# Kernel tuning notes

Measured on AMD Instinct MI355X. Metric: run time of the kernel, lower is better.

Reference implementation:

```python
import jax, jax.numpy as jnp
import numpy as np

B, S, N, F, H, O = 4, 16, 1024, 64, 128, 64
L_LAYERS, N_HEADS, CHUNK = 3, 4, 128
EPS = 1e-5


def setup_inputs() -> dict:
    key = jax.random.key(0)
    ks = jax.random.split(key, 16)
    adj = (jax.random.uniform(ks[0], (B, S, N, N)) < 0.05).astype(jnp.float32)
    adj = adj * (1.0 - jnp.eye(N, dtype=jnp.float32))
    x = jax.random.normal(ks[1], (B, S, F), dtype=jnp.float32)
    mask = jnp.ones((B, S), dtype=jnp.float32)
    sd = lambda fan_in: 1.0 / np.sqrt(fan_in)
    inp = {
        "x": x, "adj": adj, "mask": mask,
        "feature_importance": jnp.ones((F,), jnp.float32),
        "W_in": jax.random.normal(ks[2], (F, H)) * sd(F),
        "b_in": jnp.zeros((H,), jnp.float32),
        "ln_g": jnp.ones((H,), jnp.float32),
        "ln_b": jnp.zeros((H,), jnp.float32),
        "gcn_W": jax.random.normal(ks[3], (L_LAYERS, H, H)) * sd(H),
        "gcn_b": jnp.zeros((L_LAYERS, H), jnp.float32),
        "bn_g": jnp.ones((L_LAYERS, H), jnp.float32),
        "bn_b": jnp.zeros((L_LAYERS, H), jnp.float32),
        "Wqkv": jax.random.normal(ks[4], (3 * H, H)) * sd(H),
        "bqkv": jnp.zeros((3 * H,), jnp.float32),
        "Wo": jax.random.normal(ks[5], (H, H)) * sd(H),
        "bo": jnp.zeros((H,), jnp.float32),
        "W_out": jax.random.normal(ks[6], (H, O)) * sd(H),
        "b_out": jnp.zeros((O,), jnp.float32),
    }
    return inp


def _chunked_mha(h, Wqkv, bqkv, Wo, bo):
    # h: [B,S,N,H]; attention within chunks of CHUNK nodes (torch MHA, eval mode)
    b, s, n, hdim = h.shape
    c, dh = n // CHUNK, hdim // N_HEADS
    xr = h.reshape(b, s, c, CHUNK, hdim)
    qkv = xr @ Wqkv.T + bqkv                      # [B,S,C,L,3H]
    q, k, v = jnp.split(qkv, 3, axis=-1)
    split = lambda t: t.reshape(b, s, c, CHUNK, N_HEADS, dh).swapaxes(-3, -2)  # [B,S,C,nh,L,dh]
    q, k, v = split(q) * (dh ** -0.5), split(k), split(v)
    attn = jax.nn.softmax(jnp.einsum('bscnld,bscnmd->bscnlm', q, k), axis=-1)
    o = jnp.einsum('bscnlm,bscnmd->bscnld', attn, v)
    o = o.swapaxes(-3, -2).reshape(b, s, c, CHUNK, hdim) @ Wo.T + bo
    return o.reshape(b, s, n, hdim)


def reference(x, adj, mask, feature_importance, W_in, b_in, ln_g, ln_b,
              gcn_W, gcn_b, bn_g, bn_b, Wqkv, bqkv, Wo, bo, W_out, b_out):
    b, s, f = x.shape
    n = adj.shape[-1]
    # feature scaling + input projection + layer norm (same vector for all nodes)
    xv = (x * feature_importance) @ W_in + b_in            # [B,S,H]
    mu = xv.mean(-1, keepdims=True)
    var = ((xv - mu) ** 2).mean(-1, keepdims=True)
    hv = (xv - mu) / jnp.sqrt(var + EPS) * ln_g + ln_b
    h = jnp.broadcast_to(hv[:, :, None, :], (b, s, n, hv.shape[-1]))  # [B,S,N,H]
    h_init = h
    # GCN normalization: D^{-1/2} (A + I) D^{-1/2}
    A_hat = adj + jnp.eye(n, dtype=adj.dtype)
    dinv = jax.lax.rsqrt(A_hat.sum(-1))                     # [B,S,N]
    A_norm = dinv[..., :, None] * A_hat * dinv[..., None, :]
    bn_scale = 1.0 / np.sqrt(1.0 + EPS)  # eval BN, running mean 0 / var 1
    for l in range(L_LAYERS):
        hw = h @ gcn_W[l]
        hc = jnp.einsum('bsnm,bsmh->bsnh', A_norm, hw) + gcn_b[l]
        hc = hc * bn_scale * bn_g[l] + bn_b[l]
        hc = _chunked_mha(hc, Wqkv, bqkv, Wo, bo)
        hc = jax.nn.relu(hc)  # dropout = identity in eval
        h = h + hc            # use_skip (num_layers > 1)
    h = h + h_init
    node_embeddings = h @ W_out + b_out                    # [B,S,N,O]
    graph_embeddings = node_embeddings.mean(axis=2)        # [B,S,O]
    graph_embeddings = graph_embeddings * mask[:, :, None]
    node_embeddings = node_embeddings * mask[:, :, None, None]
    return node_embeddings, graph_embeddings
```

## Files before the change

### kernel.cpp

```cpp
#include <hip/hip_runtime.h>

typedef __bf16 bf16_t;
typedef bf16_t bf16x8 __attribute__((ext_vector_type(8)));
typedef float f32x4 __attribute__((ext_vector_type(4)));

#define DEV static __device__ __forceinline__

constexpr float kBnScale = 0.999995000037499375f;

DEV unsigned short f2bf(float f) {
  unsigned u = __builtin_bit_cast(unsigned, f);
  u += 0x7fffu + ((u >> 16) & 1u);
  return (unsigned short)(u >> 16);
}
DEV float bf2f(unsigned short s) {
  return __builtin_bit_cast(float, ((unsigned)s) << 16);
}
DEV f32x4 mfma16(bf16x8 a, bf16x8 b, f32x4 c) {
  return __builtin_amdgcn_mfma_f32_16x16x32_bf16(a, b, c, 0, 0, 0);
}
DEV unsigned swz(unsigned byteoff, unsigned row) { return byteoff ^ ((row & 7u) << 4); }

__global__ __launch_bounds__(256) void k_pre(
    const float* __restrict__ adj, unsigned short* __restrict__ cols,
    int* __restrict__ cnt, float* __restrict__ dinv,
    const float* __restrict__ x, const float* __restrict__ fi,
    const float* __restrict__ Win, const float* __restrict__ bin,
    const float* __restrict__ lng, const float* __restrict__ lnb,
    const float* __restrict__ gW, const float* __restrict__ bng,
    float* __restrict__ hv, float* __restrict__ hw0s,
    const float* __restrict__ Wqkv, const float* __restrict__ Wo,
    const float* __restrict__ Wout,
    unsigned short* __restrict__ WqkvB, unsigned short* __restrict__ WoB,
    unsigned short* __restrict__ gWB, unsigned short* __restrict__ WoutB) {
  const int bid = blockIdx.x;
  if (bid < 16384) {
    const int c4 = (bid & 7) * 2048 + (bid >> 3);
    const int w = threadIdx.x >> 6, lane = threadIdx.x & 63;
    const long row = (long)c4 * 4 + w;
    const float* ap = adj + row * 1024;
    unsigned short* cp = cols + row * 128;
    int c = 0;
#pragma unroll
    for (int it = 0; it < 4; ++it) {
      const float4 v4 = *(const float4*)(ap + it * 256 + lane * 4);
      const float vv[4] = {v4.x, v4.y, v4.z, v4.w};
#pragma unroll
      for (int j = 0; j < 4; ++j) {
        const unsigned long long m = __ballot(vv[j] != 0.0f);
        const int pos = c + __popcll(m & ((1ull << lane) - 1ull));
        if (vv[j] != 0.0f && pos < 128) cp[pos] = (unsigned short)(it * 256 + lane * 4 + j);
        c += __popcll(m);
      }
    }
    if (lane == 0) {
      cnt[row] = c;
      dinv[row] = 1.0f / sqrtf((float)(c + 1));
    }
  } else if (bid < 16448) {
    __shared__ float sred[2], sred2[2], shv[128];
    const int bs = bid - 16384, t = threadIdx.x;
    float accv = 0.f, d = 0.f;
    if (t < 128) {
      accv = bin[t];
      for (int f = 0; f < 64; ++f) accv += x[bs * 64 + f] * fi[f] * Win[f * 128 + t];
      float ssum = accv;
      for (int m = 1; m < 64; m <<= 1) ssum += __shfl_xor(ssum, m);
      if ((t & 63) == 0) sred[t >> 6] = ssum;
    }
    __syncthreads();
    const float mu = (sred[0] + sred[1]) * (1.0f / 128.0f);
    if (t < 128) {
      d = accv - mu;
      float vs = d * d;
      for (int m = 1; m < 64; m <<= 1) vs += __shfl_xor(vs, m);
      if ((t & 63) == 0) sred2[t >> 6] = vs;
    }
    __syncthreads();
    const float var = (sred2[0] + sred2[1]) * (1.0f / 128.0f);
    if (t < 128) {
      const float h = d / sqrtf(var + 1e-5f) * lng[t] + lnb[t];
      hv[bs * 128 + t] = h;
      shv[t] = h;
    }
    __syncthreads();
    if (t < 128) {
      float a2 = 0.f;
      for (int k = 0; k < 128; ++k) a2 += shv[k] * gW[k * 128 + t];
      hw0s[bs * 128 + t] = a2 * kBnScale * bng[t];
    }
  } else {
    const int i = (bid - 16448) * 256 + threadIdx.x;
    if (i < 49152) {
      WqkvB[i] = f2bf(Wqkv[i]);
    } else if (i < 65536) {
      const int j = i - 49152;
      WoB[j] = f2bf(Wo[j]);
    } else if (i < 114688) {
      const int j = i - 65536, l = j >> 14, r = j & 16383, n = r >> 7, k = r & 127;
      gWB[j] = f2bf(gW[(l << 14) + k * 128 + n]);
    } else {
      const int j = i - 114688, n = j >> 7, k = j & 127;
      WoutB[j] = f2bf(Wout[k * 64 + n]);
    }
  }
}

__global__ __launch_bounds__(256) void k_scal2(const unsigned short* __restrict__ cols,
                                               const int* __restrict__ cnt, const float* __restrict__ dinv,
                                               const float* __restrict__ hw0s,
                                               const float* __restrict__ gb0, const float* __restrict__ bng0,
                                               const float* __restrict__ bnb0,
                                               unsigned* __restrict__ hc0) {
  int b = blockIdx.x;
  b = (b & 7) * 2048 + (b >> 3);
  const int w = threadIdx.x >> 6, lane = threadIdx.x & 63;
  const long row = (long)b * 4 + w;
  const int cn = cnt[row] < 128 ? cnt[row] : 128;
  const long bsbase = row & ~1023L;
  const int c0 = cols[row * 128 + lane];
  const int c1 = cols[row * 128 + 64 + lane];
  float s = 0.f;
  if (lane < cn) s += dinv[bsbase + c0];
  if (lane + 64 < cn) s += dinv[bsbase + c1];
  for (int m = 1; m < 64; m <<= 1) s += __shfl_xor(s, m);
  const float d = dinv[row];
  const float S = d * (d + s);
  const int bs = (int)(row >> 10);
  const float2 hw = ((const float2*)hw0s)[bs * 64 + lane];
  const float2 g2 = ((const float2*)gb0)[lane];
  const float2 bg = ((const float2*)bng0)[lane];
  const float2 bb = ((const float2*)bnb0)[lane];
  const float v0 = S * hw.x + (g2.x * kBnScale * bg.x + bb.x);
  const float v1 = S * hw.y + (g2.y * kBnScale * bg.y + bb.y);
  hc0[row * 64 + lane] = (unsigned)f2bf(v0) | ((unsigned)f2bf(v1) << 16);
}

__global__ __launch_bounds__(256) void k_qkv(const unsigned short* __restrict__ hc,
                                             const unsigned short* __restrict__ WqkvB,
                                             const float* __restrict__ bqkv,
                                             unsigned short* __restrict__ qkvb) {
  __shared__ __align__(16) unsigned short Ab[128 * 128];
  __shared__ __align__(16) unsigned short Bb[128 * 128];
  const int t = threadIdx.x;
  const int cx = (blockIdx.x & 7) * 64 + (blockIdx.x >> 3);
  const long blockRow = (long)cx * 128;
  const int pan = blockIdx.y;

#pragma unroll
  for (int i = 0; i < 8; ++i) {
    const int f = (t + i * 256) * 8;
    const unsigned row = f >> 7, k = f & 127;
    *(uint4*)(Ab + (swz(row * 256u + k * 2u, row) >> 1)) = *(const uint4*)(hc + blockRow * 128 + f);
    const unsigned n = row;
    *(uint4*)(Bb + (swz(n * 256u + k * 2u, n) >> 1)) = *(const uint4*)(WqkvB + pan * 16384 + f);
  }
  __syncthreads();

  const int lane = t & 63, w = t >> 6, wr = w >> 1, wc = w & 1;
  const f32x4 vzero = {0.f, 0.f, 0.f, 0.f};
  f32x4 acc[4][4];
#pragma unroll
  for (int a = 0; a < 4; ++a)
#pragma unroll
    for (int b = 0; b < 4; ++b) acc[a][b] = vzero;
#pragma unroll
  for (int kk = 0; kk < 4; ++kk) {
    const unsigned kb = kk * 64u + (unsigned)((lane >> 4) << 4);
    bf16x8 af[4], bfr[4];
#pragma unroll
    for (int mt = 0; mt < 4; ++mt) {
      const unsigned row = wr * 64 + mt * 16 + (lane & 15);
      af[mt] = *(const bf16x8*)(Ab + (swz(row * 256u + kb, row) >> 1));
    }
#pragma unroll
    for (int nt = 0; nt < 4; ++nt) {
      const unsigned col = wc * 64 + nt * 16 + (lane & 15);
      bfr[nt] = *(const bf16x8*)(Bb + (swz(col * 256u + kb, col) >> 1));
    }
#pragma unroll
    for (int mt = 0; mt < 4; ++mt)
#pragma unroll
      for (int nt = 0; nt < 4; ++nt) acc[mt][nt] = mfma16(af[mt], bfr[nt], acc[mt][nt]);
  }
#pragma unroll
  for (int mt = 0; mt < 4; ++mt)
#pragma unroll
    for (int nt = 0; nt < 4; ++nt)
#pragma unroll
      for (int r = 0; r < 4; ++r) {
        const long gRow = blockRow + wr * 64 + mt * 16 + ((lane >> 4) << 2) + r;
        const int gCol = wc * 64 + nt * 16 + (lane & 15);
        qkvb[gRow * 384 + pan * 128 + gCol] = f2bf(acc[mt][nt][r] + bqkv[pan * 128 + gCol]);
      }
}

__global__ __launch_bounds__(256) void k_spmm(const uint4* __restrict__ hwp16,
                                              const unsigned short* __restrict__ cols,
                                              const int* __restrict__ cnt, const float* __restrict__ dinv,
                                              const float* __restrict__ gb, const float* __restrict__ bng,
                                              const float* __restrict__ bnb, uint4* __restrict__ hc16) {
  int b = blockIdx.x;
  b = (b & 7) * 2048 + (b >> 3);
  const int w = threadIdx.x >> 6, lane = threadIdx.x & 63;
  const int g = lane >> 4, l15 = lane & 15;
  const long row = (long)b * 4 + w;
  __shared__ unsigned short scol[4][128];
  scol[w][lane] = cols[row * 128 + lane];
  scol[w][lane + 64] = cols[row * 128 + 64 + lane];
  const int cn = cnt[row] < 128 ? cnt[row] : 128;
  const long bsbase = row & ~1023L;
  float acc[8];
#pragma unroll
  for (int e = 0; e < 8; ++e) acc[e] = 0.f;
  if (g == 0) {
    const uint4 u = hwp16[row * 16 + l15];
    const unsigned uu[4] = {u.x, u.y, u.z, u.w};
#pragma unroll
    for (int e2 = 0; e2 < 4; ++e2) {
      acc[e2 * 2] += bf2f((unsigned short)uu[e2]);
      acc[e2 * 2 + 1] += bf2f((unsigned short)(uu[e2] >> 16));
    }
  }
  const int cn4 = cn & ~3;
#pragma unroll 2
  for (int i = 0; i < cn4; i += 4) {
    const int j = scol[w][i + g];
    const uint4 u = hwp16[(bsbase + j) * 16 + l15];
    const unsigned uu[4] = {u.x, u.y, u.z, u.w};
#pragma unroll
    for (int e2 = 0; e2 < 4; ++e2) {
      acc[e2 * 2] += bf2f((unsigned short)uu[e2]);
      acc[e2 * 2 + 1] += bf2f((unsigned short)(uu[e2] >> 16));
    }
  }
  if (cn4 + g < cn) {
    const int j = scol[w][cn4 + g];
    const uint4 u = hwp16[(bsbase + j) * 16 + l15];
    const unsigned uu[4] = {u.x, u.y, u.z, u.w};
#pragma unroll
    for (int e2 = 0; e2 < 4; ++e2) {
      acc[e2 * 2] += bf2f((unsigned short)uu[e2]);
      acc[e2 * 2 + 1] += bf2f((unsigned short)(uu[e2] >> 16));
    }
  }
#pragma unroll
  for (int e = 0; e < 8; ++e) {
    acc[e] += __shfl_xor(acc[e], 16);
    acc[e] += __shfl_xor(acc[e], 32);
  }
  if (g == 0) {
    const float di = dinv[row];
    const float4 gv0 = ((const float4*)gb)[l15 * 2], gv1 = ((const float4*)gb)[l15 * 2 + 1];
    const float4 bg0 = ((const float4*)bng)[l15 * 2], bg1 = ((const float4*)bng)[l15 * 2 + 1];
    const float4 bb0 = ((const float4*)bnb)[l15 * 2], bb1 = ((const float4*)bnb)[l15 * 2 + 1];
    float o[8];
    o[0] = (di * acc[0] + gv0.x) * (kBnScale * bg0.x) + bb0.x;
    o[1] = (di * acc[1] + gv0.y) * (kBnScale * bg0.y) + bb0.y;
    o[2] = (di * acc[2] + gv0.z) * (kBnScale * bg0.z) + bb0.z;
    o[3] = (di * acc[3] + gv0.w) * (kBnScale * bg0.w) + bb0.w;
    o[4] = (di * acc[4] + gv1.x) * (kBnScale * bg1.x) + bb1.x;
    o[5] = (di * acc[5] + gv1.y) * (kBnScale * bg1.y) + bb1.y;
    o[6] = (di * acc[6] + gv1.z) * (kBnScale * bg1.z) + bb1.z;
    o[7] = (di * acc[7] + gv1.w) * (kBnScale * bg1.w) + bb1.w;
    uint4 r;
    r.x = (unsigned)f2bf(o[0]) | ((unsigned)f2bf(o[1]) << 16);
    r.y = (unsigned)f2bf(o[2]) | ((unsigned)f2bf(o[3]) << 16);
    r.z = (unsigned)f2bf(o[4]) | ((unsigned)f2bf(o[5]) << 16);
    r.w = (unsigned)f2bf(o[6]) | ((unsigned)f2bf(o[7]) << 16);
    hc16[row * 16 + l15] = r;
  }
}

template <int MODE>
__global__ __launch_bounds__(256, 2) void k_af(
    const unsigned short* __restrict__ qkv,
    const unsigned short* __restrict__ WoB, const unsigned short* __restrict__ B2,
    const float* __restrict__ bo, const float* __restrict__ hv,
    const float* __restrict__ dinv, const float* __restrict__ bout,
    const float* __restrict__ mask,
    float* __restrict__ hbuf, unsigned short* __restrict__ hwp,
    float* __restrict__ ne, float* __restrict__ gpart) {
  __shared__ __align__(16) unsigned short sm[32768];
  unsigned short* Ab = sm;
  unsigned short* Bb = sm + 16384;
  const int t = threadIdx.x, lane = t & 63, hd = t >> 6;
  const int g = lane >> 4, l15 = lane & 15;
  const int c = (blockIdx.x & 7) * 64 + (blockIdx.x >> 3);
  const long cb = (long)c * 128;
  const int bs = (int)(cb >> 10);
  const f32x4 vzero = {0.f, 0.f, 0.f, 0.f};

  {
    const int m = t >> 1, half = t & 1;
    const unsigned short* vrow = qkv + (cb + m) * 384 + 256 + half * 64;
#pragma unroll
    for (int c8 = 0; c8 < 8; ++c8) {
      const uint4 u = *(const uint4*)(vrow + c8 * 8);
      const int col0 = half * 64 + c8 * 8;
      unsigned short* vb = Ab + (col0 >> 5) * 4096;
      const int dh0 = col0 & 31;
      const unsigned short e[8] = {(unsigned short)u.x, (unsigned short)(u.x >> 16),
                                   (unsigned short)u.y, (unsigned short)(u.y >> 16),
                                   (unsigned short)u.z, (unsigned short)(u.z >> 16),
                                   (unsigned short)u.w, (unsigned short)(u.w >> 16)};
#pragma unroll
      for (int j = 0; j < 8; ++j) {
        const unsigned dh = dh0 + j;
        vb[swz(dh * 256u + (unsigned)m * 2u, dh) >> 1] = e[j];
      }
    }
  }
  bf16x8 kf[8];
#pragma unroll
  for (int nt = 0; nt < 8; ++nt)
    kf[nt] = *(const bf16x8*)(qkv + (cb + nt * 16 + l15) * 384 + 128 + hd * 32 + (g << 3));
  __syncthreads();

  const unsigned short* vbb = Ab + hd * 4096;
  unsigned short* pb = Bb + hd * 4096;
  const float SC = 0.17677669529663687f * 1.4426950408889634f;
  unsigned pk[4][2][2][2];

#pragma unroll 1
  for (int p = 0; p < 4; ++p) {
    bf16x8 qf[2];
#pragma unroll
    for (int mt = 0; mt < 2; ++mt)
      qf[mt] = *(const bf16x8*)(qkv + (cb + p * 32 + mt * 16 + l15) * 384 + hd * 32 + (g << 3));
    f32x4 s[2][8];
#pragma unroll
    for (int mt = 0; mt < 2; ++mt)
#pragma unroll
      for (int nt = 0; nt < 8; ++nt) s[mt][nt] = vzero;
#pragma unroll
    for (int nt = 0; nt < 8; ++nt)
#pragma unroll
      for (int mt = 0; mt < 2; ++mt) s[mt][nt] = mfma16(qf[mt], kf[nt], s[mt][nt]);

    float rinv[2][4];
#pragma unroll
    for (int mt = 0; mt < 2; ++mt) {
#pragma unroll
      for (int r = 0; r < 4; ++r) {
        float mx = s[mt][0][r];
#pragma unroll
        for (int nt = 1; nt < 8; ++nt) mx = fmaxf(mx, s[mt][nt][r]);
#pragma unroll
        for (int msk = 1; msk < 16; msk <<= 1) mx = fmaxf(mx, __shfl_xor(mx, msk));
        const unsigned qp = mt * 16 + g * 4 + r;
        float sum = 0.f;
#pragma unroll
        for (int nt = 0; nt < 8; ++nt) {
          const float e = exp2f((s[mt][nt][r] - mx) * SC);
          sum += e;
          pb[swz(qp * 256u + (nt * 16 + l15) * 2u, qp) >> 1] = f2bf(e);
        }
#pragma unroll
        for (int msk = 1; msk < 16; msk <<= 1) sum += __shfl_xor(sum, msk);
        rinv[mt][r] = 1.0f / sum;
      }
    }

    f32x4 o[2][2];
#pragma unroll
    for (int mt = 0; mt < 2; ++mt)
#pragma unroll
      for (int nt = 0; nt < 2; ++nt) o[mt][nt] = vzero;
#pragma unroll
    for (int kk = 0; kk < 4; ++kk) {
      const unsigned kb = kk * 64u + (unsigned)(g << 4);
      bf16x8 pa[2], vf[2];
#pragma unroll
      for (int mt = 0; mt < 2; ++mt) {
        const unsigned rq = mt * 16 + l15;
        pa[mt] = *(const bf16x8*)(pb + (swz(rq * 256u + kb, rq) >> 1));
      }
#pragma unroll
      for (int nt = 0; nt < 2; ++nt) {
        const unsigned dh = nt * 16 + l15;
        vf[nt] = *(const bf16x8*)(vbb + (swz(dh * 256u + kb, dh) >> 1));
      }
#pragma unroll
      for (int mt = 0; mt < 2; ++mt)
#pragma unroll
        for (int nt = 0; nt < 2; ++nt) o[mt][nt] = mfma16(pa[mt], vf[nt], o[mt][nt]);
    }
#pragma unroll
    for (int mt = 0; mt < 2; ++mt)
#pragma unroll
      for (int nt = 0; nt < 2; ++nt) {
        pk[p][mt][nt][0] = (unsigned)f2bf(o[mt][nt][0] * rinv[mt][0]) |
                           ((unsigned)f2bf(o[mt][nt][1] * rinv[mt][1]) << 16);
        pk[p][mt][nt][1] = (unsigned)f2bf(o[mt][nt][2] * rinv[mt][2]) |
                           ((unsigned)f2bf(o[mt][nt][3] * rinv[mt][3]) << 16);
      }
  }
  __syncthreads();

#pragma unroll
  for (int p = 0; p < 4; ++p)
#pragma unroll
    for (int mt = 0; mt < 2; ++mt)
#pragma unroll
      for (int nt = 0; nt < 2; ++nt)
#pragma unroll
        for (int rr = 0; rr < 2; ++rr) {
          const unsigned u = pk[p][mt][nt][rr];
          const unsigned row0 = p * 32 + mt * 16 + g * 4 + rr * 2;
          const unsigned col = hd * 32 + nt * 16 + l15;
          Ab[swz(row0 * 256u + col * 2u, row0) >> 1] = (unsigned short)u;
          Ab[swz((row0 + 1) * 256u + col * 2u, row0 + 1) >> 1] = (unsigned short)(u >> 16);
        }
#pragma unroll
  for (int i = 0; i < 8; ++i) {
    const int f = (t + i * 256) * 8;
    const unsigned n = f >> 7, k = f & 127;
    *(uint4*)(Bb + (swz(n * 256u + k * 2u, n) >> 1)) = *(const uint4*)(WoB + f);
  }
  __syncthreads();

  const int wr = hd >> 1, wc = hd & 1;
  f32x4 acc[4][4];
#pragma unroll
  for (int a = 0; a < 4; ++a)
#pragma unroll
    for (int b = 0; b < 4; ++b) acc[a][b] = vzero;
#pragma unroll
  for (int kk = 0; kk < 4; ++kk) {
    const unsigned kb = kk * 64u + (unsigned)(g << 4);
    bf16x8 af[4], bfr[4];
#pragma unroll
    for (int mt = 0; mt < 4; ++mt) {
      const unsigned row = wr * 64 + mt * 16 + l15;
      af[mt] = *(const bf16x8*)(Ab + (swz(row * 256u + kb, row) >> 1));
    }
#pragma unroll
    for (int nt = 0; nt < 4; ++nt) {
      const unsigned col = wc * 64 + nt * 16 + l15;
      bfr[nt] = *(const bf16x8*)(Bb + (swz(col * 256u + kb, col) >> 1));
    }
#pragma unroll
    for (int mt = 0; mt < 4; ++mt)
#pragma unroll
      for (int nt = 0; nt < 4; ++nt) acc[mt][nt] = mfma16(af[mt], bfr[nt], acc[mt][nt]);
  }
  __syncthreads();

  {
    const float b0 = bo[wc * 64 + l15], b1 = bo[wc * 64 + 16 + l15];
    const float b2c = bo[wc * 64 + 32 + l15], b3c = bo[wc * 64 + 48 + l15];
    const float bb[4] = {b0, b1, b2c, b3c};
    float hb[4];
#pragma unroll
    for (int nt = 0; nt < 4; ++nt) hb[nt] = hv[bs * 128 + wc * 64 + nt * 16 + l15];
#pragma unroll
    for (int mt = 0; mt < 4; ++mt)
#pragma unroll
      for (int nt = 0; nt < 4; ++nt)
#pragma unroll
        for (int r = 0; r < 4; ++r) {
          const unsigned row = wr * 64 + mt * 16 + g * 4 + r;
          const long gRow = cb + row;
          const unsigned col = wc * 64 + nt * 16 + l15;
          float v = acc[mt][nt][r] + bb[nt];
          v = v > 0.f ? v : 0.f;
          if constexpr (MODE == 0) {
            v += hb[nt];
          } else {
            v += hbuf[gRow * 128 + col];
            if constexpr (MODE == 2) v += hb[nt];
          }
          if constexpr (MODE < 2) hbuf[gRow * 128 + col] = v;
          Ab[swz(row * 256u + col * 2u, row) >> 1] = f2bf(v);
        }
  }
  if constexpr (MODE < 2) {
#pragma unroll
    for (int i = 0; i < 8; ++i) {
      const int f = (t + i * 256) * 8;
      const unsigned n = f >> 7, k = f & 127;
      *(uint4*)(Bb + (swz(n * 256u + k * 2u, n) >> 1)) = *(const uint4*)(B2 + f);
    }
  } else {
#pragma unroll
    for (int i = 0; i < 4; ++i) {
      const int f = (t + i * 256) * 8;
      const unsigned n = f >> 7, k = f & 127;
      *(uint4*)(Bb + (swz(n * 256u + k * 2u, n) >> 1)) = *(const uint4*)(B2 + f);
    }
  }
  __syncthreads();

  if constexpr (MODE < 2) {
#pragma unroll
    for (int a = 0; a < 4; ++a)
#pragma unroll
      for (int b = 0; b < 4; ++b) acc[a][b] = vzero;
#pragma unroll
    for (int kk = 0; kk < 4; ++kk) {
      const unsigned kb = kk * 64u + (unsigned)(g << 4);
      bf16x8 af[4], bfr[4];
#pragma unroll
      for (int mt = 0; mt < 4; ++mt) {
        const unsigned row = wr * 64 + mt * 16 + l15;
        af[mt] = *(const bf16x8*)(Ab + (swz(row * 256u + kb, row) >> 1));
      }
#pragma unroll
      for (int nt = 0; nt < 4; ++nt) {
        const unsigned col = wc * 64 + nt * 16 + l15;
        bfr[nt] = *(const bf16x8*)(Bb + (swz(col * 256u + kb, col) >> 1));
      }
#pragma unroll
      for (int mt = 0; mt < 4; ++mt)
#pragma unroll
        for (int nt = 0; nt < 4; ++nt) acc[mt][nt] = mfma16(af[mt], bfr[nt], acc[mt][nt]);
    }
#pragma unroll
    for (int mt = 0; mt < 4; ++mt)
#pragma unroll
      for (int nt = 0; nt < 4; ++nt)
#pragma unroll
        for (int r = 0; r < 4; ++r) {
          const long gRow = cb + wr * 64 + mt * 16 + g * 4 + r;
          const unsigned col = wc * 64 + nt * 16 + l15;
          hwp[gRow * 128 + col] = f2bf(acc[mt][nt][r] * dinv[gRow]);
        }
  } else {
    f32x4 acc2[4][2];
#pragma unroll
    for (int a = 0; a < 4; ++a)
#pragma unroll
      for (int b = 0; b < 2; ++b) acc2[a][b] = vzero;
#pragma unroll
    for (int kk = 0; kk < 4; ++kk) {
      const unsigned kb = kk * 64u + (unsigned)(g << 4);
      bf16x8 af[4], bfr[2];
#pragma unroll
      for (int mt = 0; mt < 4; ++mt) {
        const unsigned row = wr * 64 + mt * 16 + l15;
        af[mt] = *(const bf16x8*)(Ab + (swz(row * 256u + kb, row) >> 1));
      }
#pragma unroll
      for (int nt = 0; nt < 2; ++nt) {
        const unsigned col = wc * 32 + nt * 16 + l15;
        bfr[nt] = *(const bf16x8*)(Bb + (swz(col * 256u + kb, col) >> 1));
      }
#pragma unroll
      for (int mt = 0; mt < 4; ++mt)
#pragma unroll
        for (int nt = 0; nt < 2; ++nt) acc2[mt][nt] = mfma16(af[mt], bfr[nt], acc2[mt][nt]);
    }
    const float mk = mask[bs];
#pragma unroll
    for (int nt = 0; nt < 2; ++nt) {
      const unsigned col = wc * 32 + nt * 16 + l15;
      const float b2 = bout[col];
      float csum = 0.f;
#pragma unroll
      for (int mt = 0; mt < 4; ++mt)
#pragma unroll
        for (int r = 0; r < 4; ++r) {
          const long gRow = cb + wr * 64 + mt * 16 + g * 4 + r;
          const float v = (acc2[mt][nt][r] + b2) * mk;
          ne[gRow * 64 + col] = v;
          csum += v;
        }
      csum += __shfl_xor(csum, 16);
      csum += __shfl_xor(csum, 32);
      if (g == 0) gpart[((long)c * 2 + wr) * 64 + col] = csum;
    }
  }
}

__global__ void k_gfin(const float* __restrict__ gpart, float* __restrict__ ge) {
  const int tid = blockIdx.x * 256 + threadIdx.x;
  if (tid >= 4096) return;
  const int bs = tid >> 6, col = tid & 63;
  float s = 0.f;
#pragma unroll
  for (int q = 0; q < 16; ++q) s += gpart[(bs * 16 + q) * 64 + col];
  ge[tid] = s * (1.0f / 1024.0f);
}

extern "C" void kernel_launch(void* const* d_in, const int* in_sizes, int n_in,
                              void* d_out, int out_size, void* d_ws, size_t ws_size,
                              hipStream_t stream) {
  const float* x = (const float*)d_in[0];
  const float* adj = (const float*)d_in[1];
  const float* mask = (const float*)d_in[2];
  const float* fi = (const float*)d_in[3];
  const float* Win = (const float*)d_in[4];
  const float* bin = (const float*)d_in[5];
  const float* lng = (const float*)d_in[6];
  const float* lnb = (const float*)d_in[7];
  const float* gW = (const float*)d_in[8];
  const float* gB = (const float*)d_in[9];
  const float* bng = (const float*)d_in[10];
  const float* bnb = (const float*)d_in[11];
  const float* Wqkv = (const float*)d_in[12];
  const float* bqkv = (const float*)d_in[13];
  const float* Wo = (const float*)d_in[14];
  const float* bo = (const float*)d_in[15];
  const float* Wout = (const float*)d_in[16];
  const float* bout = (const float*)d_in[17];

  char* ws = (char*)d_ws;
  float* dinv = (float*)ws;                    ws += 65536 * 4;
  int* cnt = (int*)ws;                         ws += 65536 * 4;
  float* hv = (float*)ws;                      ws += 64 * 128 * 4;
  float* hw0s = (float*)ws;                    ws += 64 * 128 * 4;
  float* gpart = (float*)ws;                   ws += 1024 * 64 * 4;
  unsigned short* WqkvB = (unsigned short*)ws; ws += 49152 * 2;
  unsigned short* WoB = (unsigned short*)ws;   ws += 16384 * 2;
  unsigned short* gWB = (unsigned short*)ws;   ws += 49152 * 2;
  unsigned short* WoutB = (unsigned short*)ws; ws += 8192 * 2;
  unsigned short* cols = (unsigned short*)ws;  ws += (size_t)65536 * 128 * 2;
  float* hbuf = (float*)ws;                    ws += (size_t)65536 * 128 * 4;
  unsigned short* hwp = (unsigned short*)ws;   ws += (size_t)65536 * 128 * 2;
  unsigned short* hc = (unsigned short*)ws;    ws += (size_t)65536 * 128 * 2;
  unsigned short* qkvb = (unsigned short*)ws;  ws += (size_t)65536 * 384 * 2;

  float* ne = (float*)d_out;
  float* ge = ne + (size_t)4194304;

  k_pre<<<16928, 256, 0, stream>>>(adj, cols, cnt, dinv, x, fi, Win, bin, lng, lnb,
                                   gW, bng, hv, hw0s, Wqkv, Wo, Wout,
                                   WqkvB, WoB, gWB, WoutB);
  k_scal2<<<16384, 256, 0, stream>>>(cols, cnt, dinv, hw0s, gB, bng, bnb, (unsigned*)hc);

  k_qkv<<<dim3(512, 3), 256, 0, stream>>>(hc, WqkvB, bqkv, qkvb);
  k_af<0><<<512, 256, 0, stream>>>(qkvb, WoB, gWB + 16384, bo, hv, dinv, nullptr, nullptr,
                                   hbuf, hwp, nullptr, nullptr);
  k_spmm<<<16384, 256, 0, stream>>>((const uint4*)hwp, cols, cnt, dinv,
                                    gB + 128, bng + 128, bnb + 128, (uint4*)hc);
  k_qkv<<<dim3(512, 3), 256, 0, stream>>>(hc, WqkvB, bqkv, qkvb);
  k_af<1><<<512, 256, 0, stream>>>(qkvb, WoB, gWB + 32768, bo, hv, dinv, nullptr, nullptr,
                                   hbuf, hwp, nullptr, nullptr);
  k_spmm<<<16384, 256, 0, stream>>>((const uint4*)hwp, cols, cnt, dinv,
                                    gB + 256, bng + 256, bnb + 256, (uint4*)hc);
  k_qkv<<<dim3(512, 3), 256, 0, stream>>>(hc, WqkvB, bqkv, qkvb);
  k_af<2><<<512, 256, 0, stream>>>(qkvb, WoB, WoutB, bo, hv, dinv, bout, mask,
                                   hbuf, nullptr, ne, gpart);

  k_gfin<<<16, 256, 0, stream>>>(gpart, ge);
}
```

Measured before the change: 349.8 us.

## Fuse sparse aggregation into QKV GEMM and store residual in bf16

The separate scalar/SpMM kernels that wrote the aggregated hidden state to global memory are merged into the QKV projection kernel. Each block now gathers neighbour rows for its 128-node chunk straight into shared memory, then loops over the three Q/K/V panels, which removes the hc round trip and two launches per layer. The residual buffer is also stored in bf16 instead of fp32, halving its traffic at some cost in accuracy. In exchange, the gather now runs in only 512 blocks of 4 waves, each wave handling 32 rows serially, which lowers the parallelism available to hide gather latency.

```diff
diff --git a/kernel.cpp b/kernel.cpp
--- a/kernel.cpp
+++ b/kernel.cpp
@@ -106,169 +106,170 @@
   }
 }
 
-__global__ __launch_bounds__(256) void k_scal2(const unsigned short* __restrict__ cols,
-                                               const int* __restrict__ cnt, const float* __restrict__ dinv,
-                                               const float* __restrict__ hw0s,
-                                               const float* __restrict__ gb0, const float* __restrict__ bng0,
-                                               const float* __restrict__ bnb0,
-                                               unsigned* __restrict__ hc0) {
-  int b = blockIdx.x;
-  b = (b & 7) * 2048 + (b >> 3);
-  const int w = threadIdx.x >> 6, lane = threadIdx.x & 63;
-  const long row = (long)b * 4 + w;
-  const int cn = cnt[row] < 128 ? cnt[row] : 128;
-  const long bsbase = row & ~1023L;
-  const int c0 = cols[row * 128 + lane];
-  const int c1 = cols[row * 128 + 64 + lane];
-  float s = 0.f;
-  if (lane < cn) s += dinv[bsbase + c0];
-  if (lane + 64 < cn) s += dinv[bsbase + c1];
-  for (int m = 1; m < 64; m <<= 1) s += __shfl_xor(s, m);
-  const float d = dinv[row];
-  const float S = d * (d + s);
-  const int bs = (int)(row >> 10);
-  const float2 hw = ((const float2*)hw0s)[bs * 64 + lane];
-  const float2 g2 = ((const float2*)gb0)[lane];
-  const float2 bg = ((const float2*)bng0)[lane];
-  const float2 bb = ((const float2*)bnb0)[lane];
-  const float v0 = S * hw.x + (g2.x * kBnScale * bg.x + bb.x);
-  const float v1 = S * hw.y + (g2.y * kBnScale * bg.y + bb.y);
-  hc0[row * 64 + lane] = (unsigned)f2bf(v0) | ((unsigned)f2bf(v1) << 16);
-}
-
-__global__ __launch_bounds__(256) void k_qkv(const unsigned short* __restrict__ hc,
-                                             const unsigned short* __restrict__ WqkvB,
-                                             const float* __restrict__ bqkv,
-                                             unsigned short* __restrict__ qkvb) {
+template <int GMODE>
+__global__ __launch_bounds__(256, 2) void k_qkvA(
+    const unsigned short* __restrict__ cols, const int* __restrict__ cnt,
+    const float* __restrict__ dinv, const uint4* __restrict__ hwp16,
+    const float* __restrict__ hw0s,
+    const float* __restrict__ gb, const float* __restrict__ bng, const float* __restrict__ bnb,
+    const unsigned short* __restrict__ WqkvB, const float* __restrict__ bqkv,
+    unsigned short* __restrict__ qkvb) {
   __shared__ __align__(16) unsigned short Ab[128 * 128];
   __shared__ __align__(16) unsigned short Bb[128 * 128];
-  const int t = threadIdx.x;
-  const int cx = (blockIdx.x & 7) * 64 + (blockIdx.x >> 3);
-  const long blockRow = (long)cx * 128;
-  const int pan = blockIdx.y;
-
-#pragma unroll
-  for (int i = 0; i < 8; ++i) {
-    const int f = (t + i * 256) * 8;
-    const unsigned row = f >> 7, k = f & 127;
-    *(uint4*)(Ab + (swz(row * 256u + k * 2u, row) >> 1)) = *(const uint4*)(hc + blockRow * 128 + f);
-    const unsigned n = row;
-    *(uint4*)(Bb + (swz(n * 256u + k * 2u, n) >> 1)) = *(const uint4*)(WqkvB + pan * 16384 + f);
+  const int t = threadIdx.x, lane = t & 63, w = t >> 6;
+  const int g = lane >> 4, l15 = lane & 15;
+  const int c = (blockIdx.x & 7) * 64 + (blockIdx.x >> 3);
+  const long cb = (long)c * 128;
+  const int bs = (int)(cb >> 10);
+  const long bsbase = (long)bs << 10;
+
+  for (int rr = 0; rr < 32; ++rr) {
+    const int rowl = w * 32 + rr;
+    const long row = cb + rowl;
+    const unsigned colreg = ((const unsigned*)(cols + row * 128))[lane];
+    const int cn = min(cnt[row], 128);
+    const float di = dinv[row];
+
+    if constexpr (GMODE == 0) {
+      float s = 0.f;
+      if (2 * lane < cn) s += dinv[bsbase + (colreg & 0xffffu)];
+      if (2 * lane + 1 < cn) s += dinv[bsbase + (colreg >> 16)];
+      for (int m = 1; m < 64; m <<= 1) s += __shfl_xor(s, m);
+      const float S = di * (di + s);
+      if (g == 0) {
+        const float4 hw0 = ((const float4*)(hw0s + bs * 128))[l15 * 2];
+        const float4 hw1 = ((const float4*)(hw0s + bs * 128))[l15 * 2 + 1];
+        const float4 gv0 = ((const float4*)gb)[l15 * 2], gv1 = ((const float4*)gb)[l15 * 2 + 1];
+        const float4 bg0 = ((const float4*)bng)[l15 * 2], bg1 = ((const float4*)bng)[l15 * 2 + 1];
+        const float4 bb0 = ((const float4*)bnb)[l15 * 2], bb1 = ((const float4*)bnb)[l15 * 2 + 1];
+        float o[8];
+        o[0] = S * hw0.x + (gv0.x * kBnScale * bg0.x + bb0.x);
+        o[1] = S * hw0.y + (gv0.y * kBnScale * bg0.y + bb0.y);
+        o[2] = S * hw0.z + (gv0.z * kBnScale * bg0.z + bb0.z);
+        o[3] = S * hw0.w + (gv0.w * kBnScale * bg0.w + bb0.w);
+        o[4] = S * hw1.x + (gv1.x * kBnScale * bg1.x + bb1.x);
+        o[5] = S * hw1.y + (gv1.y * kBnScale * bg1.y + bb1.y);
+        o[6] = S * hw1.z + (gv1.z * kBnScale * bg1.z + bb1.z);
+        o[7] = S * hw1.w + (gv1.w * kBnScale * bg1.w + bb1.w);
+        uint4 rbits;
+        rbits.x = (unsigned)f2bf(o[0]) | ((unsigned)f2bf(o[1]) << 16);
+        rbits.y = (unsigned)f2bf(o[2]) | ((unsigned)f2bf(o[3]) << 16);
+        rbits.z = (unsigned)f2bf(o[4]) | ((unsigned)f2bf(o[5]) << 16);
+        rbits.w = (unsigned)f2bf(o[6]) | ((unsigned)f2bf(o[7]) << 16);
+        *(uint4*)(Ab + (swz((unsigned)rowl * 256u + (unsigned)l15 * 16u, rowl) >> 1)) = rbits;
+      }
+    } else {
+      float acc[8];
+#pragma unroll
+      for (int e = 0; e < 8; ++e) acc[e] = 0.f;
+      if (g == 0) {
+        const uint4 u = hwp16[row * 16 + l15];
+        const unsigned uu[4] = {u.x, u.y, u.z, u.w};
+#pragma unroll
+        for (int e2 = 0; e2 < 4; ++e2) {
+          acc[e2 * 2] += bf2f((unsigned short)uu[e2]);
+          acc[e2 * 2 + 1] += bf2f((unsigned short)(uu[e2] >> 16));
+        }
+      }
+      const int cn4 = cn & ~3;
+#pragma unroll 2
+      for (int i = 0; i < cn4; i += 4) {
+        const unsigned jp = __shfl(colreg, (i + g) >> 1);
+        const int j = (g & 1) ? (int)(jp >> 16) : (int)(jp & 0xffffu);
+        const uint4 u = hwp16[(bsbase + j) * 16 + l15];
+        const unsigned uu[4] = {u.x, u.y, u.z, u.w};
+#pragma unroll
+        for (int e2 = 0; e2 < 4; ++e2) {
+          acc[e2 * 2] += bf2f((unsigned short)uu[e2]);
+          acc[e2 * 2 + 1] += bf2f((unsigned short)(uu[e2] >> 16));
+        }
+      }
+      if (cn4 + g < cn) {
+        const unsigned jp = __shfl(colreg, (cn4 + g) >> 1);
+        const int j = (g & 1) ? (int)(jp >> 16) : (int)(jp & 0xffffu);
+        const uint4 u = hwp16[(bsbase + j) * 16 + l15];
+        const unsigned uu[4] = {u.x, u.y, u.z, u.w};
+#pragma unroll
+        for (int e2 = 0; e2 < 4; ++e2) {
+          acc[e2 * 2] += bf2f((unsigned short)uu[e2]);
+          acc[e2 * 2 + 1] += bf2f((unsigned short)(uu[e2] >> 16));
+        }
+      }
+#pragma unroll
+      for (int e = 0; e < 8; ++e) {
+        acc[e] += __shfl_xor(acc[e], 16);
+        acc[e] += __shfl_xor(acc[e], 32);
+      }
+      if (g == 0) {
+        const float4 gv0 = ((const float4*)gb)[l15 * 2], gv1 = ((const float4*)gb)[l15 * 2 + 1];
+        const float4 bg0 = ((const float4*)bng)[l15 * 2], bg1 = ((const float4*)bng)[l15 * 2 + 1];
+        const float4 bb0 = ((const float4*)bnb)[l15 * 2], bb1 = ((const float4*)bnb)[l15 * 2 + 1];
+        float o[8];
+        o[0] = (di * acc[0] + gv0.x) * (kBnScale * bg0.x) + bb0.x;
+        o[1] = (di * acc[1] + gv0.y) * (kBnScale * bg0.y) + bb0.y;
+        o[2] = (di * acc[2] + gv0.z) * (kBnScale * bg0.z) + bb0.z;
+        o[3] = (di * acc[3] + gv0.w) * (kBnScale * bg0.w) + bb0.w;
+        o[4] = (di * acc[4] + gv1.x) * (kBnScale * bg1.x) + bb1.x;
+        o[5] = (di * acc[5] + gv1.y) * (kBnScale * bg1.y) + bb1.y;
+        o[6] = (di * acc[6] + gv1.z) * (kBnScale * bg1.z) + bb1.z;
+        o[7] = (di * acc[7] + gv1.w) * (kBnScale * bg1.w) + bb1.w;
+        uint4 rbits;
+        rbits.x = (unsigned)f2bf(o[0]) | ((unsigned)f2bf(o[1]) << 16);
+        rbits.y = (unsigned)f2bf(o[2]) | ((unsigned)f2bf(o[3]) << 16);
+        rbits.z = (unsigned)f2bf(o[4]) | ((unsigned)f2bf(o[5]) << 16);
+        rbits.w = (unsigned)f2bf(o[6]) | ((unsigned)f2bf(o[7]) << 16);
+        *(uint4*)(Ab + (swz((unsigned)rowl * 256u + (unsigned)l15 * 16u, rowl) >> 1)) = rbits;
+      }
+    }
   }
   __syncthreads();
 
-  const int lane = t & 63, w = t >> 6, wr = w >> 1, wc = w & 1;
+  const int wr = w >> 1, wc = w & 1;
   const f32x4 vzero = {0.f, 0.f, 0.f, 0.f};
-  f32x4 acc[4][4];
-#pragma unroll
-  for (int a = 0; a < 4; ++a)
-#pragma unroll
-    for (int b = 0; b < 4; ++b) acc[a][b] = vzero;
-#pragma unroll
-  for (int kk = 0; kk < 4; ++kk) {
-    const unsigned kb = kk * 64u + (unsigned)((lane >> 4) << 4);
-    bf16x8 af[4], bfr[4];
-#pragma unroll
-    for (int mt = 0; mt < 4; ++mt) {
-      const unsigned row = wr * 64 + mt * 16 + (lane & 15);
-      af[mt] = *(const bf16x8*)(Ab + (swz(row * 256u + kb, row) >> 1));
-    }
-#pragma unroll
-    for (int nt = 0; nt < 4; ++nt) {
-      const unsigned col = wc * 64 + nt * 16 + (lane & 15);
-      bfr[nt] = *(const bf16x8*)(Bb + (swz(col * 256u + kb, col) >> 1));
+#pragma unroll 1
+  for (int pan = 0; pan < 3; ++pan) {
+#pragma unroll
+    for (int i = 0; i < 8; ++i) {
+      const int f = (t + i * 256) * 8;
+      const unsigned n = f >> 7, k = f & 127;
+      *(uint4*)(Bb + (swz(n * 256u + k * 2u, n) >> 1)) = *(const uint4*)(WqkvB + pan * 16384 + f);
+    }
+    __syncthreads();
+    f32x4 acc[4][4];
+#pragma unroll
+    for (int a = 0; a < 4; ++a)
+#pragma unroll
+      for (int b = 0; b < 4; ++b) acc[a][b] = vzero;
+#pragma unroll
+    for (int kk = 0; kk < 4; ++kk) {
+      const unsigned kb = kk * 64u + (unsigned)(g << 4);
+      bf16x8 af[4], bfr[4];
+#pragma unroll
+      for (int mt = 0; mt < 4; ++mt) {
+        const unsigned row = wr * 64 + mt * 16 + l15;
+        af[mt] = *(const bf16x8*)(Ab + (swz(row * 256u + kb, row) >> 1));
+      }
+#pragma unroll
+      for (int nt = 0; nt < 4; ++nt) {
+        const unsigned col = wc * 64 + nt * 16 + l15;
+        bfr[nt] = *(const bf16x8*)(Bb + (swz(col * 256u + kb, col) >> 1));
+      }
+#pragma unroll
+      for (int mt = 0; mt < 4; ++mt)
+#pragma unroll
+        for (int nt = 0; nt < 4; ++nt) acc[mt][nt] = mfma16(af[mt], bfr[nt], acc[mt][nt]);
     }
 #pragma unroll
     for (int mt = 0; mt < 4; ++mt)
 #pragma unroll
-      for (int nt = 0; nt < 4; ++nt) acc[mt][nt] = mfma16(af[mt], bfr[nt], acc[mt][nt]);
-  }
-#pragma unroll
-  for (int mt = 0; mt < 4; ++mt)
-#pragma unroll
-    for (int nt = 0; nt < 4; ++nt)
-#pragma unroll
-      for (int r = 0; r < 4; ++r) {
-        const long gRow = blockRow + wr * 64 + mt * 16 + ((lane >> 4) << 2) + r;
-        const int gCol = wc * 64 + nt * 16 + (lane & 15);
-        qkvb[gRow * 384 + pan * 128 + gCol] = f2bf(acc[mt][nt][r] + bqkv[pan * 128 + gCol]);
-      }
-}
-
-__global__ __launch_bounds__(256) void k_spmm(const uint4* __restrict__ hwp16,
-                                              const unsigned short* __restrict__ cols,
-                                              const int* __restrict__ cnt, const float* __restrict__ dinv,
-                                              const float* __restrict__ gb, const float* __restrict__ bng,
-                                              const float* __restrict__ bnb, uint4* __restrict__ hc16) {
-  int b = blockIdx.x;
-  b = (b & 7) * 2048 + (b >> 3);
-  const int w = threadIdx.x >> 6, lane = threadIdx.x & 63;
-  const int g = lane >> 4, l15 = lane & 15;
-  const long row = (long)b * 4 + w;
-  __shared__ unsigned short scol[4][128];
-  scol[w][lane] = cols[row * 128 + lane];
-  scol[w][lane + 64] = cols[row * 128 + 64 + lane];
-  const int cn = cnt[row] < 128 ? cnt[row] : 128;
-  const long bsbase = row & ~1023L;
-  float acc[8];
-#pragma unroll
-  for (int e = 0; e < 8; ++e) acc[e] = 0.f;
-  if (g == 0) {
-    const uint4 u = hwp16[row * 16 + l15];
-    const unsigned uu[4] = {u.x, u.y, u.z, u.w};
-#pragma unroll
-    for (int e2 = 0; e2 < 4; ++e2) {
-      acc[e2 * 2] += bf2f((unsigned short)uu[e2]);
-      acc[e2 * 2 + 1] += bf2f((unsigned short)(uu[e2] >> 16));
-    }
-  }
-  const int cn4 = cn & ~3;
-#pragma unroll 2
-  for (int i = 0; i < cn4; i += 4) {
-    const int j = scol[w][i + g];
-    const uint4 u = hwp16[(bsbase + j) * 16 + l15];
-    const unsigned uu[4] = {u.x, u.y, u.z, u.w};
-#pragma unroll
-    for (int e2 = 0; e2 < 4; ++e2) {
-      acc[e2 * 2] += bf2f((unsigned short)uu[e2]);
-      acc[e2 * 2 + 1] += bf2f((unsigned short)(uu[e2] >> 16));
-    }
-  }
-  if (cn4 + g < cn) {
-    const int j = scol[w][cn4 + g];
-    const uint4 u = hwp16[(bsbase + j) * 16 + l15];
-    const unsigned uu[4] = {u.x, u.y, u.z, u.w};
-#pragma unroll
-    for (int e2 = 0; e2 < 4; ++e2) {
-      acc[e2 * 2] += bf2f((unsigned short)uu[e2]);
-      acc[e2 * 2 + 1] += bf2f((unsigned short)(uu[e2] >> 16));
-    }
-  }
-#pragma unroll
-  for (int e = 0; e < 8; ++e) {
-    acc[e] += __shfl_xor(acc[e], 16);
-    acc[e] += __shfl_xor(acc[e], 32);
-  }
-  if (g == 0) {
-    const float di = dinv[row];
-    const float4 gv0 = ((const float4*)gb)[l15 * 2], gv1 = ((const float4*)gb)[l15 * 2 + 1];
-    const float4 bg0 = ((const float4*)bng)[l15 * 2], bg1 = ((const float4*)bng)[l15 * 2 + 1];
-    const float4 bb0 = ((const float4*)bnb)[l15 * 2], bb1 = ((const float4*)bnb)[l15 * 2 + 1];
-    float o[8];
-    o[0] = (di * acc[0] + gv0.x) * (kBnScale * bg0.x) + bb0.x;
-    o[1] = (di * acc[1] + gv0.y) * (kBnScale * bg0.y) + bb0.y;
-    o[2] = (di * acc[2] + gv0.z) * (kBnScale * bg0.z) + bb0.z;
-    o[3] = (di * acc[3] + gv0.w) * (kBnScale * bg0.w) + bb0.w;
-    o[4] = (di * acc[4] + gv1.x) * (kBnScale * bg1.x) + bb1.x;
-    o[5] = (di * acc[5] + gv1.y) * (kBnScale * bg1.y) + bb1.y;
-    o[6] = (di * acc[6] + gv1.z) * (kBnScale * bg1.z) + bb1.z;
-    o[7] = (di * acc[7] + gv1.w) * (kBnScale * bg1.w) + bb1.w;
-    uint4 r;
-    r.x = (unsigned)f2bf(o[0]) | ((unsigned)f2bf(o[1]) << 16);
-    r.y = (unsigned)f2bf(o[2]) | ((unsigned)f2bf(o[3]) << 16);
-    r.z = (unsigned)f2bf(o[4]) | ((unsigned)f2bf(o[5]) << 16);
-    r.w = (unsigned)f2bf(o[6]) | ((unsigned)f2bf(o[7]) << 16);
-    hc16[row * 16 + l15] = r;
+      for (int nt = 0; nt < 4; ++nt)
+#pragma unroll
+        for (int r = 0; r < 4; ++r) {
+          const long gRow = cb + wr * 64 + mt * 16 + g * 4 + r;
+          const int gCol = wc * 64 + nt * 16 + l15;
+          qkvb[gRow * 384 + pan * 128 + gCol] = f2bf(acc[mt][nt][r] + bqkv[pan * 128 + gCol]);
+        }
+    __syncthreads();
   }
 }
 
@@ -279,7 +280,7 @@
     const float* __restrict__ bo, const float* __restrict__ hv,
     const float* __restrict__ dinv, const float* __restrict__ bout,
     const float* __restrict__ mask,
-    float* __restrict__ hbuf, unsigned short* __restrict__ hwp,
+    unsigned short* __restrict__ hbufb, unsigned short* __restrict__ hwp,
     float* __restrict__ ne, float* __restrict__ gpart) {
   __shared__ __align__(16) unsigned short sm[32768];
   unsigned short* Ab = sm;
@@ -468,11 +469,12 @@
           if constexpr (MODE == 0) {
             v += hb[nt];
           } else {
-            v += hbuf[gRow * 128 + col];
+            v += bf2f(hbufb[gRow * 128 + col]);
             if constexpr (MODE == 2) v += hb[nt];
           }
-          if constexpr (MODE < 2) hbuf[gRow * 128 + col] = v;
-          Ab[swz(row * 256u + col * 2u, row) >> 1] = f2bf(v);
+          const unsigned short vb = f2bf(v);
+          if constexpr (MODE < 2) hbufb[gRow * 128 + col] = vb;
+          Ab[swz(row * 256u + col * 2u, row) >> 1] = vb;
         }
   }
   if constexpr (MODE < 2) {
@@ -616,9 +618,8 @@
   unsigned short* gWB = (unsigned short*)ws;   ws += 49152 * 2;
   unsigned short* WoutB = (unsigned short*)ws; ws += 8192 * 2;
   unsigned short* cols = (unsigned short*)ws;  ws += (size_t)65536 * 128 * 2;
-  float* hbuf = (float*)ws;                    ws += (size_t)65536 * 128 * 4;
+  unsigned short* hbufb = (unsigned short*)ws; ws += (size_t)65536 * 128 * 2;
   unsigned short* hwp = (unsigned short*)ws;   ws += (size_t)65536 * 128 * 2;
-  unsigned short* hc = (unsigned short*)ws;    ws += (size_t)65536 * 128 * 2;
   unsigned short* qkvb = (unsigned short*)ws;  ws += (size_t)65536 * 384 * 2;
 
   float* ne = (float*)d_out;
@@ -627,21 +628,19 @@
   k_pre<<<16928, 256, 0, stream>>>(adj, cols, cnt, dinv, x, fi, Win, bin, lng, lnb,
                                    gW, bng, hv, hw0s, Wqkv, Wo, Wout,
                                    WqkvB, WoB, gWB, WoutB);
-  k_scal2<<<16384, 256, 0, stream>>>(cols, cnt, dinv, hw0s, gB, bng, bnb, (unsigned*)hc);
-
-  k_qkv<<<dim3(512, 3), 256, 0, stream>>>(hc, WqkvB, bqkv, qkvb);
+
+  k_qkvA<0><<<512, 256, 0, stream>>>(cols, cnt, dinv, nullptr, hw0s,
+                                     gB, bng, bnb, WqkvB, bqkv, qkvb);
   k_af<0><<<512, 256, 0, stream>>>(qkvb, WoB, gWB + 16384, bo, hv, dinv, nullptr, nullptr,
-                                   hbuf, hwp, nullptr, nullptr);
-  k_spmm<<<16384, 256, 0, stream>>>((const uint4*)hwp, cols, cnt, dinv,
-                                    gB + 128, bng + 128, bnb + 128, (uint4*)hc);
-  k_qkv<<<dim3(512, 3), 256, 0, stream>>>(hc, WqkvB, bqkv, qkvb);
+                                   hbufb, hwp, nullptr, nullptr);
+  k_qkvA<1><<<512, 256, 0, stream>>>(cols, cnt, dinv, (const uint4*)hwp, nullptr,
+                                     gB + 128, bng + 128, bnb + 128, WqkvB, bqkv, qkvb);
   k_af<1><<<512, 256, 0, stream>>>(qkvb, WoB, gWB + 32768, bo, hv, dinv, nullptr, nullptr,
-                                   hbuf, hwp, nullptr, nullptr);
-  k_spmm<<<16384, 256, 0, stream>>>((const uint4*)hwp, cols, cnt, dinv,
-                                    gB + 256, bng + 256, bnb + 256, (uint4*)hc);
-  k_qkv<<<dim3(512, 3), 256, 0, stream>>>(hc, WqkvB, bqkv, qkvb);
+                                   hbufb, hwp, nullptr, nullptr);
+  k_qkvA<1><<<512, 256, 0, stream>>>(cols, cnt, dinv, (const uint4*)hwp, nullptr,
+                                     gB + 256, bng + 256, bnb + 256, WqkvB, bqkv, qkvb);
   k_af<2><<<512, 256, 0, stream>>>(qkvb, WoB, WoutB, bo, hv, dinv, bout, mask,
-                                   hbuf, nullptr, ne, gpart);
+                                   hbufb, nullptr, ne, gpart);
 
   k_gfin<<<16, 256, 0, stream>>>(gpart, ge);
 }
```

New measurement: 518.7 us. 1.48x slower.

## Split QKV into planar buffers, loop panels per block, store residual in bf16

Applied to the files above, without the earlier changes.

k_qkv now loads the hc tile once and loops over the three Wqkv panels inside one block, instead of launching a 3-wide grid that reloads the A tile for each panel. Q, K and V are written to separate planar [N,128] arrays, so the attention kernel reads contiguous 256-byte rows rather than strided 768-byte rows. The residual buffer hbuf changes from fp32 to bf16, halving its read and write traffic. In exchange, the grid has a third as many blocks, which may leave the GPU underfilled, and the residual accumulates bf16 rounding error across layers.

```diff
diff --git a/kernel.cpp b/kernel.cpp
--- a/kernel.cpp
+++ b/kernel.cpp
@@ -136,63 +136,72 @@
   hc0[row * 64 + lane] = (unsigned)f2bf(v0) | ((unsigned)f2bf(v1) << 16);
 }
 
-__global__ __launch_bounds__(256) void k_qkv(const unsigned short* __restrict__ hc,
-                                             const unsigned short* __restrict__ WqkvB,
-                                             const float* __restrict__ bqkv,
-                                             unsigned short* __restrict__ qkvb) {
+__global__ __launch_bounds__(256, 2) void k_qkv(const unsigned short* __restrict__ hc,
+                                                const unsigned short* __restrict__ WqkvB,
+                                                const float* __restrict__ bqkv,
+                                                unsigned short* __restrict__ qkvb) {
   __shared__ __align__(16) unsigned short Ab[128 * 128];
   __shared__ __align__(16) unsigned short Bb[128 * 128];
   const int t = threadIdx.x;
   const int cx = (blockIdx.x & 7) * 64 + (blockIdx.x >> 3);
   const long blockRow = (long)cx * 128;
-  const int pan = blockIdx.y;
+  const int lane = t & 63, w = t >> 6, wr = w >> 1, wc = w & 1;
+  const int g = lane >> 4, l15 = lane & 15;
+  const f32x4 vzero = {0.f, 0.f, 0.f, 0.f};
 
 #pragma unroll
   for (int i = 0; i < 8; ++i) {
     const int f = (t + i * 256) * 8;
     const unsigned row = f >> 7, k = f & 127;
     *(uint4*)(Ab + (swz(row * 256u + k * 2u, row) >> 1)) = *(const uint4*)(hc + blockRow * 128 + f);
-    const unsigned n = row;
-    *(uint4*)(Bb + (swz(n * 256u + k * 2u, n) >> 1)) = *(const uint4*)(WqkvB + pan * 16384 + f);
-  }
-  __syncthreads();
-
-  const int lane = t & 63, w = t >> 6, wr = w >> 1, wc = w & 1;
-  const f32x4 vzero = {0.f, 0.f, 0.f, 0.f};
-  f32x4 acc[4][4];
-#pragma unroll
-  for (int a = 0; a < 4; ++a)
-#pragma unroll
-    for (int b = 0; b < 4; ++b) acc[a][b] = vzero;
-#pragma unroll
-  for (int kk = 0; kk < 4; ++kk) {
-    const unsigned kb = kk * 64u + (unsigned)((lane >> 4) << 4);
-    bf16x8 af[4], bfr[4];
-#pragma unroll
-    for (int mt = 0; mt < 4; ++mt) {
-      const unsigned row = wr * 64 + mt * 16 + (lane & 15);
-      af[mt] = *(const bf16x8*)(Ab + (swz(row * 256u + kb, row) >> 1));
-    }
-#pragma unroll
-    for (int nt = 0; nt < 4; ++nt) {
-      const unsigned col = wc * 64 + nt * 16 + (lane & 15);
-      bfr[nt] = *(const bf16x8*)(Bb + (swz(col * 256u + kb, col) >> 1));
+  }
+
+#pragma unroll 1
+  for (int pan = 0; pan < 3; ++pan) {
+#pragma unroll
+    for (int i = 0; i < 8; ++i) {
+      const int f = (t + i * 256) * 8;
+      const unsigned n = f >> 7, k = f & 127;
+      *(uint4*)(Bb + (swz(n * 256u + k * 2u, n) >> 1)) = *(const uint4*)(WqkvB + pan * 16384 + f);
+    }
+    __syncthreads();
+
+    f32x4 acc[4][4];
+#pragma unroll
+    for (int a = 0; a < 4; ++a)
+#pragma unroll
+      for (int b = 0; b < 4; ++b) acc[a][b] = vzero;
+#pragma unroll
+    for (int kk = 0; kk < 4; ++kk) {
+      const unsigned kb = kk * 64u + (unsigned)(g << 4);
+      bf16x8 af[4], bfr[4];
+#pragma unroll
+      for (int mt = 0; mt < 4; ++mt) {
+        const unsigned row = wr * 64 + mt * 16 + l15;
+        af[mt] = *(const bf16x8*)(Ab + (swz(row * 256u + kb, row) >> 1));
+      }
+#pragma unroll
+      for (int nt = 0; nt < 4; ++nt) {
+        const unsigned col = wc * 64 + nt * 16 + l15;
+        bfr[nt] = *(const bf16x8*)(Bb + (swz(col * 256u + kb, col) >> 1));
+      }
+#pragma unroll
+      for (int mt = 0; mt < 4; ++mt)
+#pragma unroll
+        for (int nt = 0; nt < 4; ++nt) acc[mt][nt] = mfma16(af[mt], bfr[nt], acc[mt][nt]);
     }
 #pragma unroll
     for (int mt = 0; mt < 4; ++mt)
 #pragma unroll
-      for (int nt = 0; nt < 4; ++nt) acc[mt][nt] = mfma16(af[mt], bfr[nt], acc[mt][nt]);
-  }
-#pragma unroll
-  for (int mt = 0; mt < 4; ++mt)
-#pragma unroll
-    for (int nt = 0; nt < 4; ++nt)
-#pragma unroll
-      for (int r = 0; r < 4; ++r) {
-        const long gRow = blockRow + wr * 64 + mt * 16 + ((lane >> 4) << 2) + r;
-        const int gCol = wc * 64 + nt * 16 + (lane & 15);
-        qkvb[gRow * 384 + pan * 128 + gCol] = f2bf(acc[mt][nt][r] + bqkv[pan * 128 + gCol]);
-      }
+      for (int nt = 0; nt < 4; ++nt)
+#pragma unroll
+        for (int r = 0; r < 4; ++r) {
+          const long gRow = blockRow + wr * 64 + mt * 16 + g * 4 + r;
+          const int gCol = wc * 64 + nt * 16 + l15;
+          qkvb[(size_t)pan * 8388608 + gRow * 128 + gCol] = f2bf(acc[mt][nt][r] + bqkv[pan * 128 + gCol]);
+        }
+    __syncthreads();
+  }
 }
 
 __global__ __launch_bounds__(256) void k_spmm(const uint4* __restrict__ hwp16,
@@ -274,12 +283,12 @@
 
 template <int MODE>
 __global__ __launch_bounds__(256, 2) void k_af(
-    const unsigned short* __restrict__ qkv,
+    const unsigned short* __restrict__ qkvb,
     const unsigned short* __restrict__ WoB, const unsigned short* __restrict__ B2,
     const float* __restrict__ bo, const float* __restrict__ hv,
     const float* __restrict__ dinv, const float* __restrict__ bout,
     const float* __restrict__ mask,
-    float* __restrict__ hbuf, unsigned short* __restrict__ hwp,
+    unsigned short* __restrict__ hbufb, unsigned short* __restrict__ hwp,
     float* __restrict__ ne, float* __restrict__ gpart) {
   __shared__ __align__(16) unsigned short sm[32768];
   unsigned short* Ab = sm;
@@ -290,10 +299,13 @@
   const long cb = (long)c * 128;
   const int bs = (int)(cb >> 10);
   const f32x4 vzero = {0.f, 0.f, 0.f, 0.f};
+  const unsigned short* qp = qkvb;
+  const unsigned short* kp = qkvb + 8388608;
+  const unsigned short* vp = qkvb + 16777216;
 
   {
     const int m = t >> 1, half = t & 1;
-    const unsigned short* vrow = qkv + (cb + m) * 384 + 256 + half * 64;
+    const unsigned short* vrow = vp + (cb + m) * 128 + half * 64;
 #pragma unroll
     for (int c8 = 0; c8 < 8; ++c8) {
       const uint4 u = *(const uint4*)(vrow + c8 * 8);
@@ -314,7 +326,7 @@
   bf16x8 kf[8];
 #pragma unroll
   for (int nt = 0; nt < 8; ++nt)
-    kf[nt] = *(const bf16x8*)(qkv + (cb + nt * 16 + l15) * 384 + 128 + hd * 32 + (g << 3));
+    kf[nt] = *(const bf16x8*)(kp + (cb + nt * 16 + l15) * 128 + hd * 32 + (g << 3));
   __syncthreads();
 
   const unsigned short* vbb = Ab + hd * 4096;
@@ -327,7 +339,7 @@
     bf16x8 qf[2];
 #pragma unroll
     for (int mt = 0; mt < 2; ++mt)
-      qf[mt] = *(const bf16x8*)(qkv + (cb + p * 32 + mt * 16 + l15) * 384 + hd * 32 + (g << 3));
+      qf[mt] = *(const bf16x8*)(qp + (cb + p * 32 + mt * 16 + l15) * 128 + hd * 32 + (g << 3));
     f32x4 s[2][8];
 #pragma unroll
     for (int mt = 0; mt < 2; ++mt)
@@ -348,13 +360,13 @@
         for (int nt = 1; nt < 8; ++nt) mx = fmaxf(mx, s[mt][nt][r]);
 #pragma unroll
         for (int msk = 1; msk < 16; msk <<= 1) mx = fmaxf(mx, __shfl_xor(mx, msk));
-        const unsigned qp = mt * 16 + g * 4 + r;
+        const unsigned qpr = mt * 16 + g * 4 + r;
         float sum = 0.f;
 #pragma unroll
         for (int nt = 0; nt < 8; ++nt) {
           const float e = exp2f((s[mt][nt][r] - mx) * SC);
           sum += e;
-          pb[swz(qp * 256u + (nt * 16 + l15) * 2u, qp) >> 1] = f2bf(e);
+          pb[swz(qpr * 256u + (nt * 16 + l15) * 2u, qpr) >> 1] = f2bf(e);
         }
 #pragma unroll
         for (int msk = 1; msk < 16; msk <<= 1) sum += __shfl_xor(sum, msk);
@@ -468,11 +480,12 @@
           if constexpr (MODE == 0) {
             v += hb[nt];
           } else {
-            v += hbuf[gRow * 128 + col];
+            v += bf2f(hbufb[gRow * 128 + col]);
             if constexpr (MODE == 2) v += hb[nt];
           }
-          if constexpr (MODE < 2) hbuf[gRow * 128 + col] = v;
-          Ab[swz(row * 256u + col * 2u, row) >> 1] = f2bf(v);
+          const unsigned short vb = f2bf(v);
+          if constexpr (MODE < 2) hbufb[gRow * 128 + col] = vb;
+          Ab[swz(row * 256u + col * 2u, row) >> 1] = vb;
         }
   }
   if constexpr (MODE < 2) {
@@ -616,7 +629,7 @@
   unsigned short* gWB = (unsigned short*)ws;   ws += 49152 * 2;
   unsigned short* WoutB = (unsigned short*)ws; ws += 8192 * 2;
   unsigned short* cols = (unsigned short*)ws;  ws += (size_t)65536 * 128 * 2;
-  float* hbuf = (float*)ws;                    ws += (size_t)65536 * 128 * 4;
+  unsigned short* hbufb = (unsigned short*)ws; ws += (size_t)65536 * 128 * 2;
   unsigned short* hwp = (unsigned short*)ws;   ws += (size_t)65536 * 128 * 2;
   unsigned short* hc = (unsigned short*)ws;    ws += (size_t)65536 * 128 * 2;
   unsigned short* qkvb = (unsigned short*)ws;  ws += (size_t)65536 * 384 * 2;
@@ -629,19 +642,19 @@
                                    WqkvB, WoB, gWB, WoutB);
   k_scal2<<<16384, 256, 0, stream>>>(cols, cnt, dinv, hw0s, gB, bng, bnb, (unsigned*)hc);
 
-  k_qkv<<<dim3(512, 3), 256, 0, stream>>>(hc, WqkvB, bqkv, qkvb);
+  k_qkv<<<512, 256, 0, stream>>>(hc, WqkvB, bqkv, qkvb);
   k_af<0><<<512, 256, 0, stream>>>(qkvb, WoB, gWB + 16384, bo, hv, dinv, nullptr, nullptr,
-                                   hbuf, hwp, nullptr, nullptr);
+                                   hbufb, hwp, nullptr, nullptr);
   k_spmm<<<16384, 256, 0, stream>>>((const uint4*)hwp, cols, cnt, dinv,
                                     gB + 128, bng + 128, bnb + 128, (uint4*)hc);
-  k_qkv<<<dim3(512, 3), 256, 0, stream>>>(hc, WqkvB, bqkv, qkvb);
+  k_qkv<<<512, 256, 0, stream>>>(hc, WqkvB, bqkv, qkvb);
   k_af<1><<<512, 256, 0, stream>>>(qkvb, WoB, gWB + 32768, bo, hv, dinv, nullptr, nullptr,
-                                   hbuf, hwp, nullptr, nullptr);
+                                   hbufb, hwp, nullptr, nullptr);
   k_spmm<<<16384, 256, 0, stream>>>((const uint4*)hwp, cols, cnt, dinv,
                                     gB + 256, bng + 256, bnb + 256, (uint4*)hc);
-  k_qkv<<<dim3(512, 3), 256, 0, stream>>>(hc, WqkvB, bqkv, qkvb);
+  k_qkv<<<512, 256, 0, stream>>>(hc, WqkvB, bqkv, qkvb);
   k_af<2><<<512, 256, 0, stream>>>(qkvb, WoB, WoutB, bo, hv, dinv, bout, mask,
-                                   hbuf, nullptr, ne, gpart);
+                                   hbufb, nullptr, ne, gpart);
 
   k_gfin<<<16, 256, 0, stream>>>(gpart, ge);
 }
```

After: 348.7 us, median of 2. No clear change (-0.3%).
